# Optimization experiments

Measured on AMD Instinct MI355X. Metric: run time of the kernel, lower is better.

## Reference

```python
import jax, jax.numpy as jnp
import numpy as np

EPS = 1e-5  # BatchNorm eps; BN applied in eval mode with running_mean=0, running_var=1


def conv1x1(x, w, b=None):
    # x: [B,C,H,W], w: [O,C] -> [B,O,H,W]
    y = jnp.einsum('bchw,oc->bohw', x, w)
    if b is not None:
        y = y + b[None, :, None, None]
    return y


def bn_eval(x, gamma, beta):
    # running_mean=0, running_var=1
    scale = gamma / jnp.sqrt(1.0 + EPS)
    return x * scale[None, :, None, None] + beta[None, :, None, None]


def glnl_forward(x, mask, wt_nl, bt_nl, wp_nl, bp_nl, wt_l, bt_l, wp_l, bp_l,
                 wg_nl, bg_nl, wg_l, bg_l, wW, bW, gW, betaW, wWl, gWl, betaWl):
    B, C, H, W = x.shape
    I = wt_nl.shape[0]
    N = H * W

    # non-local branch score [B,N,N]
    th_nl = conv1x1(x, wt_nl, bt_nl).reshape(B, I, N)
    ph_nl = conv1x1(x, wp_nl, bp_nl).reshape(B, I, N)
    score_nl = jax.nn.softmax(jnp.einsum('bin,bim->bnm', th_nl, ph_nl), axis=-1)

    # local branch: mask-gated projections, score [B,N,N]
    m = mask.reshape(B, 1, N)
    th_l = conv1x1(x, wt_l, bt_l).reshape(B, I, N) * m
    ph_l = conv1x1(x, wp_l, bp_l).reshape(B, I, N) * m
    score_l = jax.nn.softmax(jnp.einsum('bin,bim->bnm', th_l, ph_l), axis=-1)

    # value projections [B,I,N]
    g_nl = conv1x1(x, wg_nl, bg_nl).reshape(B, I, N)
    g_l = conv1x1(x, wg_l, bg_l).reshape(B, I, N)

    # attention aggregation -> [B,I,H,W]
    y_nl = jnp.einsum('bnm,bim->bin', score_nl, g_nl).reshape(B, I, H, W)
    y_l = jnp.einsum('bnm,bim->bin', score_l, g_l).reshape(B, I, H, W)

    # W_local: conv1x1 (no bias) -> ReLU -> BN
    y_l = bn_eval(jax.nn.relu(conv1x1(y_l, wWl)), gWl, betaWl)

    y = y_nl + y_l
    # W: conv1x1 -> ReLU -> BN, then residual
    W_y = bn_eval(jax.nn.relu(conv1x1(y, wW, bW)), gW, betaW)
    return W_y + x


def setup_inputs() -> dict:
    key = jax.random.key(0)
    ks = jax.random.split(key, 20)
    B, C, I, H, W = 4, 128, 64, 64, 64
    s = 0.02
    inp = {
        'x': jax.random.normal(ks[0], (B, C, H, W), jnp.float32),
        'mask': (jax.random.uniform(ks[1], (B, 1, H, W)) > 0.5).astype(jnp.float32),
        'wt_nl': jax.random.normal(ks[2], (I, C)) * s, 'bt_nl': jnp.zeros((I,)),
        'wp_nl': jax.random.normal(ks[3], (I, C)) * s, 'bp_nl': jnp.zeros((I,)),
        'wt_l': jax.random.normal(ks[4], (I, C)) * s, 'bt_l': jnp.zeros((I,)),
        'wp_l': jax.random.normal(ks[5], (I, C)) * s, 'bp_l': jnp.zeros((I,)),
        'wg_nl': jax.random.normal(ks[6], (I, C)) * s, 'bg_nl': jnp.zeros((I,)),
        'wg_l': jax.random.normal(ks[7], (I, C)) * s, 'bg_l': jnp.zeros((I,)),
        'wW': jax.random.normal(ks[8], (C, I)) * s, 'bW': jnp.zeros((C,)),
        'gW': jnp.ones((C,)), 'betaW': jnp.zeros((C,)),
        'wWl': jax.random.normal(ks[9], (I, I)) * s,
        'gWl': jnp.ones((I,)), 'betaWl': jnp.zeros((I,)),
    }
    return inp


def reference(x, mask, wt_nl, bt_nl, wp_nl, bp_nl, wt_l, bt_l, wp_l, bp_l,
              wg_nl, bg_nl, wg_l, bg_l, wW, bW, gW, betaW, wWl, gWl, betaWl):
    return glnl_forward(x, mask, wt_nl, bt_nl, wp_nl, bp_nl, wt_l, bt_l, wp_l, bp_l,
                        wg_nl, bg_nl, wg_l, bg_l, wW, bW, gW, betaW, wWl, gWl, betaWl)
```

## Files before the change

### kernel.cpp

```cpp
#include <hip/hip_runtime.h>

typedef unsigned short u16;
typedef __attribute__((ext_vector_type(8))) short short8;
typedef __attribute__((ext_vector_type(4))) float floatx4;
typedef __attribute__((ext_vector_type(2))) unsigned int uint2e;

#define MFMA16(a, b, c) __builtin_amdgcn_mfma_f32_16x16x32_bf16((a), (b), (c), 0, 0, 0)
#define LOG2E 1.44269504088896340736f

#define SZ_P ((size_t)4 * 64 * 4096)

__device__ __forceinline__ float bf2f(u16 u) {
    union { unsigned int i; float f; } v; v.i = ((unsigned int)u) << 16; return v.f;
}
__device__ __forceinline__ u16 f2bf(float f) {
    union { float f; unsigned int i; } v; v.f = f;
    unsigned int r = v.i + 0x7fffu + ((v.i >> 16) & 1u);
    return (u16)(r >> 16);
}
__device__ __forceinline__ unsigned int cvtpk(float a, float b) {
    unsigned int r;
    asm("v_cvt_pk_bf16_f32 %0, %1, %2" : "=v"(r) : "v"(a), "v"(b));
    return r;
}
__device__ __forceinline__ void plswap32(unsigned int &a, unsigned int &b) {
#if __has_builtin(__builtin_amdgcn_permlane32_swap)
    uint2e r = __builtin_amdgcn_permlane32_swap(a, b, false, false);
    a = r.x; b = r.y;
#else
    asm volatile("v_permlane32_swap_b32 %0, %1" : "+v"(a), "+v"(b));
#endif
}
__device__ __forceinline__ void plswap16(unsigned int &a, unsigned int &b) {
#if __has_builtin(__builtin_amdgcn_permlane16_swap)
    uint2e r = __builtin_amdgcn_permlane16_swap(a, b, false, false);
    a = r.x; b = r.y;
#else
    asm volatile("v_permlane16_swap_b32 %0, %1" : "+v"(a), "+v"(b));
#endif
}
__device__ __forceinline__ int swz(int row, int g) {
    return row * 64 + (((g ^ (row & 7)) << 3));
}

__global__ __launch_bounds__(256) void k_prep_w(
    const float* __restrict__ w0, const float* __restrict__ w1,
    const float* __restrict__ w2, const float* __restrict__ w3,
    const float* __restrict__ w4, const float* __restrict__ w5,
    const float* __restrict__ wWl, const float* __restrict__ wW,
    u16* __restrict__ wbf)
{
    const int idx = blockIdx.x * 256 + threadIdx.x;
    float v;
    if (idx < 49152) {
        const int j = idx >> 13, off = idx & 8191;
        const float* s = (j == 0) ? w0 : (j == 1) ? w1 : (j == 2) ? w2
                       : (j == 3) ? w3 : (j == 4) ? w4 : w5;
        v = s[off];
    } else if (idx < 53248) {
        v = wWl[idx - 49152];
    } else {
        v = wW[idx - 53248];
    }
    wbf[idx] = f2bf(v);
}

__global__ __launch_bounds__(256) void k_proj(
    const float* __restrict__ x, const float* __restrict__ mask,
    const u16* __restrict__ wbf,
    const float* __restrict__ bq0f, const float* __restrict__ bk0f,
    const float* __restrict__ bv0f,
    const float* __restrict__ bq1f, const float* __restrict__ bk1f,
    const float* __restrict__ bv1f,
    u16* __restrict__ q0, u16* __restrict__ k0, u16* __restrict__ v0,
    u16* __restrict__ q1, u16* __restrict__ k1, u16* __restrict__ v1)
{
    __shared__ __align__(16) u16 xt_s[64 * 136];
    const int n0 = blockIdx.x * 64, b = blockIdx.y;
    const int br = blockIdx.z;
    const u16* wq = wbf + br * 24576;
    const u16* wk = wq + 8192;
    const u16* wv = wk + 8192;
    const float* bq = br ? bq1f : bq0f;
    const float* bk = br ? bk1f : bk0f;
    const float* bv = br ? bv1f : bv0f;
    u16* q = br ? q1 : q0;  u16* k = br ? k1 : k0;  u16* v = br ? v1 : v0;

    const int t = threadIdx.x, w = t >> 6, lane = t & 63;
    const int quad = lane >> 4, l15 = lane & 15;
    const float* xb = x + ((size_t)b << 19);

    for (int idx = t; idx < 8192; idx += 256) {
        const int c = idx >> 6, n = idx & 63;
        xt_s[n * 136 + c] = f2bf(xb[((size_t)c << 12) + n0 + n]);
    }
    __syncthreads();

    short8 ax[4];
#pragma unroll
    for (int cc = 0; cc < 4; ++cc)
        ax[cc] = *(const short8*)&xt_s[(w * 16 + l15) * 136 + quad * 8 + cc * 32];

    float mv[4] = {1.f, 1.f, 1.f, 1.f};
    if (br) {
#pragma unroll
        for (int r = 0; r < 4; ++r)
            mv[r] = mask[((size_t)b << 12) + n0 + w * 16 + quad * 4 + r];
    }

#pragma unroll
    for (int qk = 0; qk < 2; ++qk) {
        const u16* wsel = qk ? wk : wq;
        const float* bb = qk ? bk : bq;
        u16* o = qk ? k : q;
        const float qscale = qk ? 1.0f : LOG2E;
#pragma unroll
        for (int ns = 0; ns < 4; ++ns) {
            floatx4 acc = {0.f, 0.f, 0.f, 0.f};
            const u16* wp = wsel + (ns * 16 + l15) * 128 + quad * 8;
#pragma unroll
            for (int cc = 0; cc < 4; ++cc)
                acc = MFMA16(ax[cc], *(const short8*)(wp + cc * 32), acc);
            const float bias_i = bb[ns * 16 + l15];
#pragma unroll
            for (int r = 0; r < 4; ++r) {
                const float val = (acc[r] + bias_i) * mv[r] * qscale;
                o[((size_t)b << 18) + (size_t)(n0 + w * 16 + quad * 4 + r) * 64
                  + ns * 16 + l15] = f2bf(val);
            }
        }
    }

    short8 aw[4];
#pragma unroll
    for (int cc = 0; cc < 4; ++cc)
        aw[cc] = *(const short8*)(wv + (w * 16 + l15) * 128 + quad * 8 + cc * 32);
    float bvr[4];
#pragma unroll
    for (int r = 0; r < 4; ++r) bvr[r] = bv[w * 16 + quad * 4 + r];
#pragma unroll
    for (int ns = 0; ns < 4; ++ns) {
        floatx4 acc = {0.f, 0.f, 0.f, 0.f};
#pragma unroll
        for (int cc = 0; cc < 4; ++cc)
            acc = MFMA16(aw[cc],
                *(const short8*)&xt_s[(ns * 16 + l15) * 136 + quad * 8 + cc * 32], acc);
#pragma unroll
        for (int r = 0; r < 4; ++r) {
            v[((size_t)b << 18) + ((size_t)(w * 16 + quad * 4 + r) << 12)
              + n0 + ns * 16 + l15] = f2bf(acc[r] + bvr[r]);
        }
    }
}

template<int NSP>
__global__ __launch_bounds__(512, 4) void k_flash(
    const u16* __restrict__ Q0, const u16* __restrict__ K0,
    const u16* __restrict__ V0,
    const u16* __restrict__ Q1, const u16* __restrict__ K1,
    const u16* __restrict__ V1,
    u16* __restrict__ num, float* __restrict__ den)
{
    constexpr int NIT = 4096 / NSP / 64;
    constexpr int SPB = (NSP == 4) ? 2 : 3;

    __shared__ __align__(16) u16 smem[18432];

    const int flat = blockIdx.x;
    const int g = flat & ((1 << (SPB + 3)) - 1), tile = flat >> (SPB + 3);
    const int b = g >> (SPB + 1), br = (g >> SPB) & 1, sp = g & (NSP - 1);
    const int z = br * NSP + sp;
    const int qb = tile * 256;
    const size_t base = ((size_t)b << 18);
    const u16* Q = (br ? Q1 : Q0) + base;
    const u16* K = (br ? K1 : K0) + base;
    const u16* V = (br ? V1 : V0) + base;
    u16* numo = num + (size_t)z * SZ_P + base;
    float* deno = den + z * 16384 + b * 4096;

    const int t = threadIdx.x, w = t >> 6, lane = t & 63;
    const int quad = lane >> 4, l15 = lane & 15;
    const int pw = w * 32 * 72;

    const int r0 = t >> 3, cg8 = (t & 7) * 8;
    const u16* Kp0 = K + (size_t)r0 * 64 + cg8;
    const u16* Vp0 = V + ((size_t)r0 << 12) + cg8;
    const int lk0 = swz(r0, t & 7);

    short8 aq[2][2];
#pragma unroll
    for (int t2 = 0; t2 < 2; ++t2)
#pragma unroll
        for (int s = 0; s < 2; ++s)
            aq[t2][s] = *(const short8*)(Q + (size_t)(qb + w * 32 + t2 * 16 + l15) * 64
                                         + s * 32 + quad * 8);

    floatx4 oacc[4][2];
#pragma unroll
    for (int it = 0; it < 4; ++it)
#pragma unroll
        for (int t2 = 0; t2 < 2; ++t2) oacc[it][t2] = (floatx4){0.f, 0.f, 0.f, 0.f};
    float dacc[2] = {0.f, 0.f};

    const int roff = tile & (NIT - 1);
    const int m_beg = sp * (4096 / NSP);

    {
        const int m0 = m_beg + (roff << 6);
        *(short8*)&smem[lk0] = *(const short8*)(Kp0 + (size_t)m0 * 64);
        *(short8*)&smem[8192 + lk0] = *(const short8*)(Vp0 + m0);
    }

    for (int j = 0; j < NIT; ++j) {
        const int cur = j & 1;
        const u16* kt = smem + cur * 4096;
        const u16* vt = smem + 8192 + cur * 4096;
        short8 pkv, pvv;
        const bool pf = (j + 1 < NIT);
        if (pf) {
            const int mn = m_beg + (((roff + j + 1) & (NIT - 1)) << 6);
            pkv = *(const short8*)(Kp0 + (size_t)mn * 64);
            pvv = *(const short8*)(Vp0 + mn);
        }
        __syncthreads();

#pragma unroll
        for (int s = 0; s < 2; ++s) {
            unsigned int w0[2][2], w1[2][2];
#pragma unroll
            for (int mtl = 0; mtl < 2; ++mtl) {
                const int mt = s * 2 + mtl;
                const int ko = swz(mt * 16 + l15, quad);
                const short8 ka0 = *(const short8*)(kt + ko);
                const short8 ka1 = *(const short8*)(kt + (ko ^ 32));
#pragma unroll
                for (int t2 = 0; t2 < 2; ++t2) {
                    floatx4 acc = {0.f, 0.f, 0.f, 0.f};
                    acc = MFMA16(ka0, aq[t2][0], acc);
                    acc = MFMA16(ka1, aq[t2][1], acc);
                    const float e0 = __builtin_amdgcn_exp2f(acc[0]);
                    const float e1 = __builtin_amdgcn_exp2f(acc[1]);
                    const float e2 = __builtin_amdgcn_exp2f(acc[2]);
                    const float e3 = __builtin_amdgcn_exp2f(acc[3]);
                    dacc[t2] += (e0 + e1) + (e2 + e3);
                    w0[mtl][t2] = cvtpk(e0, e1);
                    w1[mtl][t2] = cvtpk(e2, e3);
                }
            }
            short8 pb[2];
#pragma unroll
            for (int t2 = 0; t2 < 2; ++t2) {
                unsigned int a0 = w0[0][t2], b0 = w0[1][t2];
                unsigned int a1 = w1[0][t2], b1 = w1[1][t2];
                plswap32(a0, b0); plswap16(a0, b0);
                plswap32(a1, b1); plswap16(a1, b1);
                union { unsigned int u[4]; short8 s8; } cv;
                cv.u[0] = a0; cv.u[1] = a1; cv.u[2] = b0; cv.u[3] = b1;
                pb[t2] = cv.s8;
            }
#pragma unroll
            for (int it = 0; it < 4; ++it) {
                const short8 va = *(const short8*)(vt + swz(it * 16 + l15, s * 4 + quad));
#pragma unroll
                for (int t2 = 0; t2 < 2; ++t2)
                    oacc[it][t2] = MFMA16(va, pb[t2], oacc[it][t2]);
            }
        }

        if (pf) {
            u16* ktn = smem + (cur ^ 1) * 4096;
            u16* vtn = smem + 8192 + (cur ^ 1) * 4096;
            *(short8*)&ktn[lk0] = pkv;
            *(short8*)&vtn[lk0] = pvv;
        }
    }

#pragma unroll
    for (int t2 = 0; t2 < 2; ++t2) {
        float d = dacc[t2];
        d += __shfl_xor(d, 16, 64);
        d += __shfl_xor(d, 32, 64);
        if (quad == 0) deno[qb + w * 32 + t2 * 16 + l15] = d;
    }

    __syncthreads();
#pragma unroll
    for (int it = 0; it < 4; ++it)
#pragma unroll
        for (int t2 = 0; t2 < 2; ++t2) {
            *(uint2*)&smem[pw + (t2 * 16 + l15) * 72 + it * 16 + quad * 4] =
                make_uint2(cvtpk(oacc[it][t2][0], oacc[it][t2][1]),
                           cvtpk(oacc[it][t2][2], oacc[it][t2][3]));
        }
    __syncthreads();
#pragma unroll
    for (int ch = t; ch < 2048; ch += 512) {
        const int row = ch >> 3, cg = ch & 7;
        *(short8*)(numo + (size_t)(qb + row) * 64 + cg * 8) =
            *(const short8*)&smem[(row >> 5) * 2304 + (row & 31) * 72 + cg * 8];
    }
}

template<int NSP>
__global__ __launch_bounds__(256) void k_epi(
    const u16* __restrict__ num, const float* __restrict__ den,
    const u16* __restrict__ wbf,
    const float* __restrict__ gWl, const float* __restrict__ betaWl,
    const float* __restrict__ bW, const float* __restrict__ gW,
    const float* __restrict__ betaW,
    const float* __restrict__ x, float* __restrict__ out)
{
    __shared__ __align__(16) u16 yl_s[32 * 72];
    __shared__ __align__(16) u16 ynl_s[32 * 72];
    __shared__ __align__(16) u16 yy_s[32 * 72];
    const int b = blockIdx.y, n0 = blockIdx.x * 32;
    const int t = threadIdx.x, w = t >> 6, lane = t & 63;
    const int quad = lane >> 4, l15 = lane & 15;
    const size_t ybase = ((size_t)b << 18) + (size_t)n0 * 64;

    {
        const int row = t >> 3, cg = t & 7;
        float dn = 0.f, dl = 0.f;
#pragma unroll
        for (int sp = 0; sp < NSP; ++sp) {
            dn += den[sp * 16384 + b * 4096 + n0 + row];
            dl += den[(NSP + sp) * 16384 + b * 4096 + n0 + row];
        }
        const float inl = 1.0f / dn, ilo = 1.0f / dl;
        float an[8] = {0, 0, 0, 0, 0, 0, 0, 0}, al[8] = {0, 0, 0, 0, 0, 0, 0, 0};
#pragma unroll
        for (int sp = 0; sp < NSP; ++sp) {
            const short8 vn = *(const short8*)(num + (size_t)sp * SZ_P + ybase + row * 64 + cg * 8);
            const short8 vl = *(const short8*)(num + (size_t)(NSP + sp) * SZ_P + ybase + row * 64 + cg * 8);
#pragma unroll
            for (int j = 0; j < 8; ++j) {
                an[j] += bf2f((u16)vn[j]);
                al[j] += bf2f((u16)vl[j]);
            }
        }
        short8 ynl8, yl8;
#pragma unroll
        for (int j = 0; j < 8; ++j) {
            ynl8[j] = (short)f2bf(an[j] * inl);
            yl8[j]  = (short)f2bf(al[j] * ilo);
        }
        *(short8*)&ynl_s[row * 72 + cg * 8] = ynl8;
        *(short8*)&yl_s[row * 72 + cg * 8] = yl8;
    }
    __syncthreads();
    const float rsq = rsqrtf(1.0f + 1e-5f);
    const u16* wblW = wbf + 49152;
    const u16* wbW  = wbf + 53248;

    {
        const short8 a0 = *(const short8*)(wblW + (w * 16 + l15) * 64 + quad * 8);
        const short8 a1 = *(const short8*)(wblW + (w * 16 + l15) * 64 + 32 + quad * 8);
        float sc[4], bt[4];
#pragma unroll
        for (int r = 0; r < 4; ++r) {
            const int io = w * 16 + quad * 4 + r;
            sc[r] = gWl[io] * rsq;
            bt[r] = betaWl[io];
        }
#pragma unroll
        for (int nh = 0; nh < 2; ++nh) {
            floatx4 acc = {0.f, 0.f, 0.f, 0.f};
            const u16* bp_ = &yl_s[(nh * 16 + l15) * 72 + quad * 8];
            acc = MFMA16(a0, *(const short8*)bp_, acc);
            acc = MFMA16(a1, *(const short8*)(bp_ + 32), acc);
#pragma unroll
            for (int r = 0; r < 4; ++r) {
                const int io = w * 16 + quad * 4 + r;
                float val = fmaxf(acc[r], 0.f) * sc[r] + bt[r];
                val += bf2f(ynl_s[(nh * 16 + l15) * 72 + io]);
                yy_s[(nh * 16 + l15) * 72 + io] = f2bf(val);
            }
        }
    }
    __syncthreads();

#pragma unroll
    for (int rb = 0; rb < 2; ++rb) {
        const int c0 = rb * 64 + w * 16;
        const short8 a0 = *(const short8*)(wbW + (c0 + l15) * 64 + quad * 8);
        const short8 a1 = *(const short8*)(wbW + (c0 + l15) * 64 + 32 + quad * 8);
        float bs[4], sc[4], bt[4];
#pragma unroll
        for (int r = 0; r < 4; ++r) {
            const int c = c0 + quad * 4 + r;
            bs[r] = bW[c];
            sc[r] = gW[c] * rsq;
            bt[r] = betaW[c];
        }
#pragma unroll
        for (int nh = 0; nh < 2; ++nh) {
            floatx4 acc = {0.f, 0.f, 0.f, 0.f};
            const u16* bp_ = &yy_s[(nh * 16 + l15) * 72 + quad * 8];
            acc = MFMA16(a0, *(const short8*)bp_, acc);
            acc = MFMA16(a1, *(const short8*)(bp_ + 32), acc);
#pragma unroll
            for (int r = 0; r < 4; ++r) {
                const int c = c0 + quad * 4 + r;
                float val = fmaxf(acc[r] + bs[r], 0.f) * sc[r] + bt[r];
                const size_t xi = ((size_t)b << 19) + ((size_t)c << 12) + n0 + nh * 16 + l15;
                out[xi] = val + x[xi];
            }
        }
    }
}

extern "C" void kernel_launch(void* const* d_in, const int* in_sizes, int n_in,
                              void* d_out, int out_size, void* d_ws, size_t ws_size,
                              hipStream_t stream) {
    const float* x      = (const float*)d_in[0];
    const float* mask   = (const float*)d_in[1];
    const float* wt_nl  = (const float*)d_in[2];  const float* bt_nl = (const float*)d_in[3];
    const float* wp_nl  = (const float*)d_in[4];  const float* bp_nl = (const float*)d_in[5];
    const float* wt_l   = (const float*)d_in[6];  const float* bt_l  = (const float*)d_in[7];
    const float* wp_l   = (const float*)d_in[8];  const float* bp_l  = (const float*)d_in[9];
    const float* wg_nl  = (const float*)d_in[10]; const float* bg_nl = (const float*)d_in[11];
    const float* wg_l   = (const float*)d_in[12]; const float* bg_l  = (const float*)d_in[13];
    const float* wW     = (const float*)d_in[14]; const float* bW    = (const float*)d_in[15];
    const float* gW     = (const float*)d_in[16]; const float* betaW = (const float*)d_in[17];
    const float* wWl    = (const float*)d_in[18]; const float* gWl   = (const float*)d_in[19];
    const float* betaWl = (const float*)d_in[20];

    const size_t need8 = ((size_t)61440 + 6 * SZ_P + 16 * SZ_P) * 2
                       + (size_t)16 * 16384 * 4;
    const int nsp = (ws_size >= need8) ? 8 : 4;

    u16* ws  = (u16*)d_ws;
    u16* wbf = ws;
    u16* q0  = wbf + 61440;
    u16* k0  = q0 + SZ_P;
    u16* v0  = k0 + SZ_P;
    u16* q1  = v0 + SZ_P;
    u16* k1  = q1 + SZ_P;
    u16* v1  = k1 + SZ_P;
    u16* num = v1 + SZ_P;
    float* den = (float*)(num + (size_t)2 * nsp * SZ_P);

    k_prep_w<<<dim3(240), 256, 0, stream>>>(wt_nl, wp_nl, wg_nl,
                                            wt_l, wp_l, wg_l, wWl, wW, wbf);
    k_proj<<<dim3(64, 4, 2), 256, 0, stream>>>(x, mask, wbf,
        bt_nl, bp_nl, bg_nl, bt_l, bp_l, bg_l,
        q0, k0, v0, q1, k1, v1);
    if (nsp == 8) {
        k_flash<8><<<dim3(1024), 512, 0, stream>>>(q0, k0, v0, q1, k1, v1, num, den);
        k_epi<8><<<dim3(128, 4), 256, 0, stream>>>(num, den, wbf, gWl, betaWl,
                                                   bW, gW, betaW, x, (float*)d_out);
    } else {
        k_flash<4><<<dim3(512), 512, 0, stream>>>(q0, k0, v0, q1, k1, v1, num, den);
        k_epi<4><<<dim3(128, 4), 256, 0, stream>>>(num, den, wbf, gWl, betaWl,
                                                   bW, gW, betaW, x, (float*)d_out);
    }
}
```

Measured before the change: 165.9 us.

## Stream K/V tiles directly into LDS with global_load_lds and raise MFMA priority

Replaces the register-staged K/V prefetch (global load into registers, then an LDS store after compute) with direct global-to-LDS loads. The XOR swizzle is now applied on the global source address, so the LDS destination is linear per wave. The loop now waits on vmcnt and barriers at the top, then issues the next tile's loads into the other buffer. It also wraps the MFMA sections in s_setprio to favour matrix issue across waves. This frees VGPRs and the LDS write instructions, but it adds a full vmcnt wait each iteration and depends on the swizzle remapping being correct.

```diff
diff --git a/kernel.cpp b/kernel.cpp
--- a/kernel.cpp
+++ b/kernel.cpp
@@ -41,6 +41,11 @@
 }
 __device__ __forceinline__ int swz(int row, int g) {
     return row * 64 + (((g ^ (row & 7)) << 3));
+}
+__device__ __forceinline__ void gload16(const void* g, void* l) {
+    __builtin_amdgcn_global_load_lds(
+        (const __attribute__((address_space(1))) unsigned char*)g,
+        (__attribute__((address_space(3))) unsigned char*)l, 16, 0, 0);
 }
 
 __global__ __launch_bounds__(256) void k_prep_w(
@@ -182,10 +187,12 @@
     const int quad = lane >> 4, l15 = lane & 15;
     const int pw = w * 32 * 72;
 
-    const int r0 = t >> 3, cg8 = (t & 7) * 8;
-    const u16* Kp0 = K + (size_t)r0 * 64 + cg8;
-    const u16* Vp0 = V + ((size_t)r0 << 12) + cg8;
-    const int lk0 = swz(r0, t & 7);
+    const int r0 = t >> 3;
+    const int gx = (t & 7) ^ ((t >> 3) & 7);
+    const u16* Kp0 = K + (size_t)r0 * 64 + gx * 8;
+    const u16* Vp0 = V + ((size_t)r0 << 12) + gx * 8;
+    u16* kw = smem + w * 512;
+    u16* vw = smem + 8192 + w * 512;
 
     short8 aq[2][2];
 #pragma unroll
@@ -207,22 +214,22 @@
 
     {
         const int m0 = m_beg + (roff << 6);
-        *(short8*)&smem[lk0] = *(const short8*)(Kp0 + (size_t)m0 * 64);
-        *(short8*)&smem[8192 + lk0] = *(const short8*)(Vp0 + m0);
+        gload16(Kp0 + (size_t)m0 * 64, kw);
+        gload16(Vp0 + m0, vw);
     }
 
     for (int j = 0; j < NIT; ++j) {
         const int cur = j & 1;
+        asm volatile("s_waitcnt vmcnt(0)" ::: "memory");
+        __builtin_amdgcn_sched_barrier(0);
+        __syncthreads();
+        if (j + 1 < NIT) {
+            const int mn = m_beg + (((roff + j + 1) & (NIT - 1)) << 6);
+            gload16(Kp0 + (size_t)mn * 64, kw + (cur ^ 1) * 4096);
+            gload16(Vp0 + mn, vw + (cur ^ 1) * 4096);
+        }
         const u16* kt = smem + cur * 4096;
         const u16* vt = smem + 8192 + cur * 4096;
-        short8 pkv, pvv;
-        const bool pf = (j + 1 < NIT);
-        if (pf) {
-            const int mn = m_beg + (((roff + j + 1) & (NIT - 1)) << 6);
-            pkv = *(const short8*)(Kp0 + (size_t)mn * 64);
-            pvv = *(const short8*)(Vp0 + mn);
-        }
-        __syncthreads();
 
 #pragma unroll
         for (int s = 0; s < 2; ++s) {
@@ -236,8 +243,10 @@
 #pragma unroll
                 for (int t2 = 0; t2 < 2; ++t2) {
                     floatx4 acc = {0.f, 0.f, 0.f, 0.f};
+                    __builtin_amdgcn_s_setprio(1);
                     acc = MFMA16(ka0, aq[t2][0], acc);
                     acc = MFMA16(ka1, aq[t2][1], acc);
+                    __builtin_amdgcn_s_setprio(0);
                     const float e0 = __builtin_amdgcn_exp2f(acc[0]);
                     const float e1 = __builtin_amdgcn_exp2f(acc[1]);
                     const float e2 = __builtin_amdgcn_exp2f(acc[2]);
@@ -258,6 +267,7 @@
                 cv.u[0] = a0; cv.u[1] = a1; cv.u[2] = b0; cv.u[3] = b1;
                 pb[t2] = cv.s8;
             }
+            __builtin_amdgcn_s_setprio(1);
 #pragma unroll
             for (int it = 0; it < 4; ++it) {
                 const short8 va = *(const short8*)(vt + swz(it * 16 + l15, s * 4 + quad));
@@ -265,13 +275,7 @@
                 for (int t2 = 0; t2 < 2; ++t2)
                     oacc[it][t2] = MFMA16(va, pb[t2], oacc[it][t2]);
             }
-        }
-
-        if (pf) {
-            u16* ktn = smem + (cur ^ 1) * 4096;
-            u16* vtn = smem + 8192 + (cur ^ 1) * 4096;
-            *(short8*)&ktn[lk0] = pkv;
-            *(short8*)&vtn[lk0] = pvv;
+            __builtin_amdgcn_s_setprio(0);
         }
     }
 
```

Result: no change. 166.5 us (+0.4%).
